# Optimization experiments

Hardware: AMD Instinct MI355X
Metric: run time of the kernel (lower is better)

Reference implementation:

```python
import jax, jax.numpy as jnp
import numpy as np
import math


def setup_inputs() -> dict:
    key = jax.random.key(0)
    ks = jax.random.split(key, 5)
    B, S, H = 4, 2048, 512
    scale = 1.0 / math.sqrt(H)
    return {
        "input_seq_rep": jax.random.normal(ks[0], (B, S, H), dtype=jnp.float32),
        "Wk": jax.random.normal(ks[1], (H, H), dtype=jnp.float32) * scale,
        "bk": jax.random.normal(ks[2], (H,), dtype=jnp.float32) * 0.01,
        "Wq": jax.random.normal(ks[3], (H, H), dtype=jnp.float32) * scale,
        "bq": jax.random.normal(ks[4], (H,), dtype=jnp.float32) * 0.01,
        "k_mul": 64,
    }


def reference(input_seq_rep, Wk, bk, Wq, bq, k_mul):
    B, S, H = input_seq_rep.shape
    x = jax.nn.relu(input_seq_rep)
    # torch Linear: y = x @ W.T + b
    k = jnp.einsum("bsh,oh->bso", x, Wk) + bk  # key (also used as value)
    q = jnp.einsum("bsh,oh->bso", x, Wq) + bq

    # local causal band mask: max(0, i - k_mul) <= j <= i
    i = jnp.arange(S)[:, None]
    j = jnp.arange(S)[None, :]
    mask = (j >= jnp.maximum(i - k_mul, 0)) & (j <= i)  # [S, S] bool

    scores = jnp.einsum("bqh,bkh->bqk", q, k) / jnp.sqrt(jnp.asarray(H, q.dtype))
    scores = jnp.where(mask[None, :, :], scores, jnp.asarray(-1e9, scores.dtype))
    attn = jax.nn.softmax(scores, axis=-1)  # [B, S, S]
    out = jnp.einsum("bqk,bkh->bqh", attn, k)  # value == key
    return out, attn
```

## Files before the change

kernel.cpp:

```cpp
#include <hip/hip_runtime.h>
#include <hip/hip_bf16.h>
#include <float.h>
#include <math.h>


typedef __attribute__((ext_vector_type(4))) float f32x4;
typedef __attribute__((ext_vector_type(8))) short short8;
typedef __attribute__((ext_vector_type(4))) short short4v;

#define TM 128
#define TN 128
#define TK 64

#define QBLK 16
#define KW 96
#define SCP 100
#define PPAD 104

static __device__ __forceinline__ short f2bf(float f) {
    __hip_bfloat16 h = __float2bfloat16(f);
    return *reinterpret_cast<short*>(&h);
}

__global__ __launch_bounds__(256) void gemm_mfma_relu_bias_bf16(
    const float* __restrict__ A,
    const float* __restrict__ Wq, const float* __restrict__ bq, short* __restrict__ Cq,
    const float* __restrict__ Wk, const float* __restrict__ bk, short* __restrict__ Ck,
    short* __restrict__ CkT, float* __restrict__ attnz, long long zPerBlk4,
    int M, int N, int K, int sshift)
{
    const float* W    = blockIdx.z ? Wk : Wq;
    const float* bias = blockIdx.z ? bk : bq;
    short*       C    = blockIdx.z ? Ck : Cq;

    __shared__ __align__(16) short lds[TM * TN];
    short* As = lds;
    short* Bs = lds + TM * TK;

    const int tid  = threadIdx.x;
    const int lane = tid & 63;
    const int wave = tid >> 6;
    const int wr   = (wave >> 1) * 64;
    const int wc   = (wave & 1) * 64;
    const int m0   = blockIdx.x * TM;
    const int n0   = blockIdx.y * TN;

    const int blkLin = blockIdx.x + gridDim.x * (blockIdx.y + gridDim.y * blockIdx.z);
    f32x4* zp = (f32x4*)attnz;
    const size_t zbase = (size_t)blkLin * (size_t)zPerBlk4;
    const int nsteps = K / TK;
    const int perStep = (int)(zPerBlk4 / ((long long)nsteps * 256));
    const f32x4 z4 = {0.f, 0.f, 0.f, 0.f};

    const int lr = lane & 15;
    const int lk = (lane >> 4) * 8;

    f32x4 acc[4][4];
    #pragma unroll
    for (int m = 0; m < 4; ++m)
        #pragma unroll
        for (int n = 0; n < 4; ++n)
            #pragma unroll
            for (int r = 0; r < 4; ++r) acc[m][n][r] = 0.f;

    for (int k0 = 0; k0 < K; k0 += TK) {
        #pragma unroll
        for (int i = 0; i < 8; ++i) {
            int f   = tid + (i << 8);
            int row = f >> 4;
            int cq  = (f & 15) << 2;
            int sidx = row * TK + (cq ^ ((row & 7) << 3));
            float4 va = *(const float4*)&A[(size_t)(m0 + row) * K + k0 + cq];
            short4v sa;
            sa.x = f2bf(fmaxf(va.x, 0.f));
            sa.y = f2bf(fmaxf(va.y, 0.f));
            sa.z = f2bf(fmaxf(va.z, 0.f));
            sa.w = f2bf(fmaxf(va.w, 0.f));
            *(short4v*)&As[sidx] = sa;
            float4 vb = *(const float4*)&W[(size_t)(n0 + row) * K + k0 + cq];
            short4v sb;
            sb.x = f2bf(vb.x);
            sb.y = f2bf(vb.y);
            sb.z = f2bf(vb.z);
            sb.w = f2bf(vb.w);
            *(short4v*)&Bs[sidx] = sb;
        }
        __syncthreads();

        #pragma unroll
        for (int kk = 0; kk < 2; ++kk) {
            short8 af[4], bf[4];
            #pragma unroll
            for (int m = 0; m < 4; ++m) {
                int r = wr + m * 16 + lr;
                af[m] = *(const short8*)&As[r * TK + ((kk * 32 + lk) ^ ((r & 7) << 3))];
            }
            #pragma unroll
            for (int n = 0; n < 4; ++n) {
                int r = wc + n * 16 + lr;
                bf[n] = *(const short8*)&Bs[r * TK + ((kk * 32 + lk) ^ ((r & 7) << 3))];
            }
            #pragma unroll
            for (int m = 0; m < 4; ++m)
                #pragma unroll
                for (int n = 0; n < 4; ++n)
                    acc[m][n] = __builtin_amdgcn_mfma_f32_16x16x32_bf16(
                        af[m], bf[n], acc[m][n], 0, 0, 0);
        }

        {
            int s = k0 / TK;
            size_t off = zbase + (size_t)s * perStep * 256 + tid;
            for (int j = 0; j < perStep; ++j)
                zp[off + (size_t)j * 256] = z4;
        }
        __syncthreads();
    }

    float bv[4];
    #pragma unroll
    for (int n = 0; n < 4; ++n) bv[n] = bias[n0 + wc + n * 16 + lr];
    const int cr = (lane >> 4) * 4;

    #pragma unroll
    for (int m = 0; m < 4; ++m)
        #pragma unroll
        for (int n = 0; n < 4; ++n) {
            int col = wc + n * 16 + lr;
            #pragma unroll
            for (int r = 0; r < 4; ++r) {
                int row = wr + m * 16 + cr + r;
                lds[row * TN + (col ^ ((row & 7) << 3))] = f2bf(acc[m][n][r] + bv[n]);
            }
        }
    __syncthreads();
    #pragma unroll
    for (int i = 0; i < 8; ++i) {
        int idx = tid + (i << 8);
        int m = idx >> 4, n8 = (idx & 15) << 3;
        short8 v = *(const short8*)&lds[m * TN + (n8 ^ ((m & 7) << 3))];
        *(short8*)&C[(size_t)(m0 + m) * N + n0 + n8] = v;
    }

    if (blockIdx.z) {
        __syncthreads();
        #pragma unroll
        for (int m = 0; m < 4; ++m)
            #pragma unroll
            for (int n = 0; n < 4; ++n) {
                int col = wc + n * 16 + lr;
                #pragma unroll
                for (int r = 0; r < 4; ++r) {
                    int row = wr + m * 16 + cr + r;
                    lds[col * TM + (row ^ ((col & 7) << 3))] = f2bf(acc[m][n][r] + bv[n]);
                }
            }
        __syncthreads();
        const int smask = (1 << sshift) - 1;
        #pragma unroll
        for (int i = 0; i < 8; ++i) {
            int idx = tid + (i << 8);
            int n = idx >> 4, m8 = (idx & 15) << 3;
            short8 v = *(const short8*)&lds[n * TM + (m8 ^ ((n & 7) << 3))];
            int gm = m0 + m8;
            int gb = gm >> sshift, s = gm & smask;
            *(short8*)&CkT[((size_t)gb * N + (n0 + n)) * (size_t)(smask + 1) + s] = v;
        }
    }
}

__global__ __launch_bounds__(512) void band_attn_mfma(
    const short* __restrict__ qbf, const short* __restrict__ kbf,
    const short* __restrict__ kT, const int* __restrict__ kmul_p,
    float* __restrict__ out, float* __restrict__ attn,
    int S, int H, float scale)
{
    __shared__ float sc[QBLK][SCP];
    __shared__ short pl[QBLK][PPAD];

    int bx = blockIdx.x;
    int tile = bx;
    if ((gridDim.x & 7) == 0) {
        int chunk = gridDim.x >> 3;
        tile = (bx & 7) * chunk + (bx >> 3);
    }

    const int i0  = tile * QBLK;
    const int b   = blockIdx.y;
    const int tid = threadIdx.x;
    const int lane = tid & 63;
    const int w    = tid >> 6;
    const int km   = kmul_p[0];
    const int jbase = max(i0 - (KW - QBLK), 0);

    const int lr = lane & 15;
    const int lk = (lane >> 4) * 8;
    const int fr = (lane >> 4) * 4;

    const short* qb = qbf + ((size_t)b * S + i0) * H;
    const short* kb = kbf + ((size_t)b * S + jbase) * H;
    if (w < 6) {
        f32x4 sacc;
        #pragma unroll
        for (int r = 0; r < 4; ++r) sacc[r] = 0.f;
        #pragma unroll
        for (int ks = 0; ks < 16; ++ks) {
            int hoff = ks * 32 + lk;
            short8 qa = *(const short8*)(qb + (size_t)lr * H + hoff);
            short8 kf = *(const short8*)(kb + (size_t)(w * 16 + lr) * H + hoff);
            sacc = __builtin_amdgcn_mfma_f32_16x16x32_bf16(qa, kf, sacc, 0, 0, 0);
        }
        int key = w * 16 + lr;
        int kg  = jbase + key;
        #pragma unroll
        for (int r = 0; r < 4; ++r) {
            int q = fr + r;
            int irow = i0 + q;
            bool ok = (kg <= irow) && (kg + km >= irow);
            sc[q][key] = ok ? sacc[r] * scale : -1e30f;
        }
    }
    __syncthreads();

    if (tid < 256) {
        int r = tid >> 4;
        int t = tid & 15;
        float v[6];
        #pragma unroll
        for (int c = 0; c < 6; ++c) v[c] = sc[r][t * 6 + c];
        float mx = -FLT_MAX;
        #pragma unroll
        for (int c = 0; c < 6; ++c) mx = fmaxf(mx, v[c]);
        mx = fmaxf(mx, __shfl_xor(mx, 1, 64));
        mx = fmaxf(mx, __shfl_xor(mx, 2, 64));
        mx = fmaxf(mx, __shfl_xor(mx, 4, 64));
        mx = fmaxf(mx, __shfl_xor(mx, 8, 64));
        float e[6], s = 0.f;
        #pragma unroll
        for (int c = 0; c < 6; ++c) { e[c] = __expf(v[c] - mx); s += e[c]; }
        s += __shfl_xor(s, 1, 64);
        s += __shfl_xor(s, 2, 64);
        s += __shfl_xor(s, 4, 64);
        s += __shfl_xor(s, 8, 64);
        float inv = __frcp_rn(s);
        #pragma unroll
        for (int c = 0; c < 6; ++c) {
            float p = e[c] * inv;
            sc[r][t * 6 + c] = p;
            pl[r][t * 6 + c] = f2bf(p);
        }
    }
    __syncthreads();

    short8 pa[3];
    #pragma unroll
    for (int ks = 0; ks < 3; ++ks)
        pa[ks] = *(const short8*)&pl[lr][ks * 32 + lk];

    const short* ktb = kT + (size_t)b * H * S;
    float* obase = out + ((size_t)b * S + i0) * H;
    #pragma unroll
    for (int nf = 0; nf < 4; ++nf) {
        int h = w * 64 + nf * 16 + lr;
        f32x4 oacc;
        #pragma unroll
        for (int r = 0; r < 4; ++r) oacc[r] = 0.f;
        #pragma unroll
        for (int ks = 0; ks < 3; ++ks) {
            short8 kf = *(const short8*)(ktb + (size_t)h * S + jbase + ks * 32 + lk);
            oacc = __builtin_amdgcn_mfma_f32_16x16x32_bf16(pa[ks], kf, oacc, 0, 0, 0);
        }
        #pragma unroll
        for (int r = 0; r < 4; ++r) {
            int q = fr + r;
            __builtin_nontemporal_store(oacc[r], obase + (size_t)q * H + h);
        }
    }

    if (tid < (KW / 4) * QBLK) {
        int r = tid / (KW / 4);
        int c = tid % (KW / 4);
        f32x4 o;
        #pragma unroll
        for (int j = 0; j < 4; ++j) o[j] = sc[r][c * 4 + j];
        *(f32x4*)(attn + ((size_t)b * S + i0 + r) * (size_t)S + jbase + c * 4) = o;
    }
}

extern "C" void kernel_launch(void* const* d_in, const int* in_sizes, int n_in,
                              void* d_out, int out_size, void* d_ws, size_t ws_size,
                              hipStream_t stream)
{
    const float* x  = (const float*)d_in[0];
    const float* Wk = (const float*)d_in[1];
    const float* bk = (const float*)d_in[2];
    const float* Wq = (const float*)d_in[3];
    const float* bq = (const float*)d_in[4];
    const int*   km = (const int*)d_in[5];

    const int H = in_sizes[2];
    const long long BS = (long long)in_sizes[0] / H;
    const long long S = ((long long)out_size - (long long)in_sizes[0]) / BS;
    const int B = (int)(BS / S);
    int sshift = 0;
    while ((1LL << sshift) < S) ++sshift;

    short* kT  = (short*)d_ws;
    short* qbf = kT + (size_t)B * H * S;
    short* kbf = qbf + (size_t)BS * H;

    float* outp  = (float*)d_out;
    float* attnp = outp + (size_t)BS * H;

    dim3 gg((unsigned)(BS / TM), (unsigned)(H / TN), 2);
    const long long nblk = (long long)gg.x * gg.y * 2;
    const long long zPerBlk4 = ((long long)B * S * S / 4) / nblk;

    gemm_mfma_relu_bias_bf16<<<gg, 256, 0, stream>>>(
        x, Wq, bq, qbf, Wk, bk, kbf, kT, attnp, zPerBlk4,
        (int)BS, H, H, sshift);

    const float scale = 1.0f / sqrtf((float)H);

    dim3 ag((unsigned)(S / QBLK), (unsigned)B);
    band_attn_mfma<<<ag, 512, 0, stream>>>(qbf, kbf, kT, km, outp, attnp,
                                           (int)S, H, scale);
}
```

Measured before the change: 49.54 us.

## Precast inputs to bf16 in a prep kernel and use nontemporal zero stores

Adds a separate kernel that applies relu to x and converts x, Wq and Wk to bf16 in workspace. The projection GEMM then loads bf16 tiles directly with 16-byte loads instead of converting fp32 per tile. This is meant to cut GEMM load bytes and conversion work, at the cost of an extra launch and an extra full pass over x. The attention-zeroing stores become nontemporal to reduce cache pollution.

```diff
diff --git a/kernel.cpp b/kernel.cpp
--- a/kernel.cpp
+++ b/kernel.cpp
@@ -22,14 +22,46 @@
     return *reinterpret_cast<short*>(&h);
 }
 
-__global__ __launch_bounds__(256) void gemm_mfma_relu_bias_bf16(
-    const float* __restrict__ A,
-    const float* __restrict__ Wq, const float* __restrict__ bq, short* __restrict__ Cq,
-    const float* __restrict__ Wk, const float* __restrict__ bk, short* __restrict__ Ck,
+__global__ __launch_bounds__(256) void prep_bf16(
+    const float* __restrict__ x, const float* __restrict__ Wq,
+    const float* __restrict__ Wk, short* __restrict__ xb,
+    short* __restrict__ wqb, short* __restrict__ wkb,
+    long long nx, long long nw)
+{
+    long long t = (long long)blockIdx.x * blockDim.x + threadIdx.x;
+    long long total8 = (nx + 2 * nw) >> 3;
+    long long stride = (long long)gridDim.x * blockDim.x;
+    for (; t < total8; t += stride) {
+        long long e = t << 3;
+        const float* src;
+        short* dst;
+        bool relu = false;
+        if (e < nx)            { src = x  + e;            dst = xb  + e;            relu = true; }
+        else if (e < nx + nw)  { src = Wq + (e - nx);      dst = wqb + (e - nx); }
+        else                   { src = Wk + (e - nx - nw); dst = wkb + (e - nx - nw); }
+        float4 a = *(const float4*)src;
+        float4 b = *(const float4*)(src + 4);
+        if (relu) {
+            a.x = fmaxf(a.x, 0.f); a.y = fmaxf(a.y, 0.f);
+            a.z = fmaxf(a.z, 0.f); a.w = fmaxf(a.w, 0.f);
+            b.x = fmaxf(b.x, 0.f); b.y = fmaxf(b.y, 0.f);
+            b.z = fmaxf(b.z, 0.f); b.w = fmaxf(b.w, 0.f);
+        }
+        short8 o;
+        o[0] = f2bf(a.x); o[1] = f2bf(a.y); o[2] = f2bf(a.z); o[3] = f2bf(a.w);
+        o[4] = f2bf(b.x); o[5] = f2bf(b.y); o[6] = f2bf(b.z); o[7] = f2bf(b.w);
+        *(short8*)dst = o;
+    }
+}
+
+__global__ __launch_bounds__(256) void gemm_mfma_bias_bf16(
+    const short* __restrict__ Ab,
+    const short* __restrict__ Wqb, const float* __restrict__ bq, short* __restrict__ Cq,
+    const short* __restrict__ Wkb, const float* __restrict__ bk, short* __restrict__ Ck,
     short* __restrict__ CkT, float* __restrict__ attnz, long long zPerBlk4,
     int M, int N, int K, int sshift)
 {
-    const float* W    = blockIdx.z ? Wk : Wq;
+    const short* Wb   = blockIdx.z ? Wkb : Wqb;
     const float* bias = blockIdx.z ? bk : bq;
     short*       C    = blockIdx.z ? Ck : Cq;
 
@@ -65,25 +97,15 @@
 
     for (int k0 = 0; k0 < K; k0 += TK) {
         #pragma unroll
-        for (int i = 0; i < 8; ++i) {
-            int f   = tid + (i << 8);
-            int row = f >> 4;
-            int cq  = (f & 15) << 2;
-            int sidx = row * TK + (cq ^ ((row & 7) << 3));
-            float4 va = *(const float4*)&A[(size_t)(m0 + row) * K + k0 + cq];
-            short4v sa;
-            sa.x = f2bf(fmaxf(va.x, 0.f));
-            sa.y = f2bf(fmaxf(va.y, 0.f));
-            sa.z = f2bf(fmaxf(va.z, 0.f));
-            sa.w = f2bf(fmaxf(va.w, 0.f));
-            *(short4v*)&As[sidx] = sa;
-            float4 vb = *(const float4*)&W[(size_t)(n0 + row) * K + k0 + cq];
-            short4v sb;
-            sb.x = f2bf(vb.x);
-            sb.y = f2bf(vb.y);
-            sb.z = f2bf(vb.z);
-            sb.w = f2bf(vb.w);
-            *(short4v*)&Bs[sidx] = sb;
+        for (int i = 0; i < 4; ++i) {
+            int idx = tid + (i << 8);
+            int row = idx >> 3;
+            int g8  = (idx & 7) << 3;
+            int sidx = row * TK + (g8 ^ ((row & 7) << 3));
+            short8 va = *(const short8*)&Ab[(size_t)(m0 + row) * K + k0 + g8];
+            *(short8*)&As[sidx] = va;
+            short8 vb = *(const short8*)&Wb[(size_t)(n0 + row) * K + k0 + g8];
+            *(short8*)&Bs[sidx] = vb;
         }
         __syncthreads();
 
@@ -112,7 +134,7 @@
             int s = k0 / TK;
             size_t off = zbase + (size_t)s * perStep * 256 + tid;
             for (int j = 0; j < perStep; ++j)
-                zp[off + (size_t)j * 256] = z4;
+                __builtin_nontemporal_store(z4, &zp[off + (size_t)j * 256]);
         }
         __syncthreads();
     }
@@ -306,18 +328,27 @@
     while ((1LL << sshift) < S) ++sshift;
 
     short* kT  = (short*)d_ws;
-    short* qbf = kT + (size_t)B * H * S;
+    short* qbf = kT  + (size_t)B * H * S;
     short* kbf = qbf + (size_t)BS * H;
+    short* xb  = kbf + (size_t)BS * H;
+    short* wqb = xb  + (size_t)BS * H;
+    short* wkb = wqb + (size_t)H * H;
 
     float* outp  = (float*)d_out;
     float* attnp = outp + (size_t)BS * H;
+
+    const long long nx = (long long)BS * H;
+    const long long nw = (long long)H * H;
+    const long long total8 = (nx + 2 * nw) >> 3;
+    unsigned pblocks = (unsigned)((total8 + 255) / 256);
+    prep_bf16<<<pblocks, 256, 0, stream>>>(x, Wq, Wk, xb, wqb, wkb, nx, nw);
 
     dim3 gg((unsigned)(BS / TM), (unsigned)(H / TN), 2);
     const long long nblk = (long long)gg.x * gg.y * 2;
     const long long zPerBlk4 = ((long long)B * S * S / 4) / nblk;
 
-    gemm_mfma_relu_bias_bf16<<<gg, 256, 0, stream>>>(
-        x, Wq, bq, qbf, Wk, bk, kbf, kT, attnp, zPerBlk4,
+    gemm_mfma_bias_bf16<<<gg, 256, 0, stream>>>(
+        xb, wqb, bq, qbf, wkb, bk, kbf, kT, attnp, zPerBlk4,
         (int)BS, H, H, sshift);
 
     const float scale = 1.0f / sqrtf((float)H);
```

Result: slower. 51.34 us (+3.6%).
